# Kernel tuning notes

Hardware: AMD Instinct MI355X
Metric: run time of the kernel (lower is better)

## Reference

```python
import jax, jax.numpy as jnp
import numpy as np

D_MODEL = 1024
N_HEAD = 16


def setup_inputs() -> dict:
    key = jax.random.key(0)
    k1, k2, k3 = jax.random.split(key, 3)
    scale = 1.0 / np.sqrt(D_MODEL)
    x = jax.random.normal(k1, (1, 4096, D_MODEL), dtype=jnp.float32)
    # nn.Linear weights stored as [out, in]; applied as x @ W.T
    w_attn = jax.random.normal(k2, (3 * D_MODEL, D_MODEL), dtype=jnp.float32) * scale
    w_proj = jax.random.normal(k3, (D_MODEL, D_MODEL), dtype=jnp.float32) * scale
    return {"x": x, "w_attn": w_attn, "w_proj": w_proj}


def reference(x, w_attn, w_proj):
    B, T, C = x.shape
    H = N_HEAD
    hd = C // H
    qkv = x @ w_attn.T                      # [B, T, 3C]
    q, k, v = jnp.split(qkv, 3, axis=-1)
    # [B, T, C] -> [B, H, T, hd]
    q = q.reshape(B, T, H, hd).transpose(0, 2, 1, 3)
    k = k.reshape(B, T, H, hd).transpose(0, 2, 1, 3)
    v = v.reshape(B, T, H, hd).transpose(0, 2, 1, 3)
    att = jnp.einsum("bhqd,bhkd->bhqk", q, k) * (1.0 / np.sqrt(hd))  # [B,H,T,T]
    causal = jnp.tril(jnp.ones((T, T), dtype=bool))
    att = jnp.where(causal[None, None], att, -jnp.inf)
    att = jax.nn.softmax(att, axis=-1)
    y = jnp.einsum("bhqk,bhkd->bhqd", att, v)  # [B,H,T,hd]
    y = y.transpose(0, 2, 1, 3).reshape(B, T, C)
    return y @ w_proj.T
```

## Files before the change

### kernel.cpp

```cpp
#include <hip/hip_runtime.h>
#include <hip/hip_bf16.h>
#include <stdint.h>

typedef __bf16 bf16x8 __attribute__((ext_vector_type(8)));
typedef float f32x4 __attribute__((ext_vector_type(4)));

#define T_SEQ 4096
#define C_DIM 1024
#define H_NUM 16
#define HD 64
#define C3 3072
#define NEG_BIG (-30000.0f)

__device__ __forceinline__ unsigned short f2bf(float f) {
    uint32_t u = __builtin_bit_cast(uint32_t, f);
    u += 0x7fffu + ((u >> 16) & 1u);
    return (unsigned short)(u >> 16);
}

__device__ __forceinline__ uint32_t pk_bf16(float a, float b) {
    __hip_bfloat162 h = __float22bfloat162_rn(float2{a, b});
    uint32_t u;
    __builtin_memcpy(&u, &h, sizeof(u));
    return u;
}

__device__ __forceinline__ bf16x8 ld_bf8(const unsigned short* p) {
    return *reinterpret_cast<const bf16x8*>(p);
}

__device__ __forceinline__ void async_g2l16(const unsigned short* g, unsigned short* l) {
    __builtin_amdgcn_global_load_lds(
        (const __attribute__((address_space(1))) void*)g,
        (__attribute__((address_space(3))) void*)l, 16, 0, 0);
}

__device__ __forceinline__ void store_c(unsigned short* C, size_t idx, float v) { C[idx] = f2bf(v); }
__device__ __forceinline__ void store_c(float* C, size_t idx, float v)          { C[idx] = v; }

__device__ __forceinline__ void cvt8(const float* src, unsigned short* dst) {
    float4 f0 = *(const float4*)src;
    float4 f1 = *(const float4*)(src + 4);
    union { uint32_t w[4]; uint4 q; } t;
    t.w[0] = pk_bf16(f0.x, f0.y);
    t.w[1] = pk_bf16(f0.z, f0.w);
    t.w[2] = pk_bf16(f1.x, f1.y);
    t.w[3] = pk_bf16(f1.z, f1.w);
    *(uint4*)dst = t.q;
}

__global__ void cvt_xw(const float* __restrict__ x, const float* __restrict__ wa,
                       unsigned short* __restrict__ xb, unsigned short* __restrict__ wab) {
    int i = (blockIdx.x * blockDim.x + threadIdx.x) * 8;
    if (i < T_SEQ * C_DIM) cvt8(x + i, xb + i);
    else {
        int k = i - T_SEQ * C_DIM;
        if (k < C3 * C_DIM) cvt8(wa + k, wab + k);
    }
}

__global__ void cvt_f32_bf16(const float* __restrict__ src, unsigned short* __restrict__ dst, int n) {
    int i = (blockIdx.x * blockDim.x + threadIdx.x) * 8;
    if (i >= n) return;
    cvt8(src + i, dst + i);
}

__global__ __launch_bounds__(256) void v_transpose(
    const unsigned short* __restrict__ qkv, unsigned short* __restrict__ Vt)
{
    __shared__ unsigned short tile[64][72];
    const int t0 = blockIdx.x * 64, c0 = blockIdx.y * 64;
    const int r = threadIdx.x >> 2, q = threadIdx.x & 3;

    const unsigned short* src = qkv + (size_t)(t0 + r) * C3 + 2 * C_DIM + c0 + q * 16;
    *(uint4*)&tile[r][q * 16]     = *(const uint4*)src;
    *(uint4*)&tile[r][q * 16 + 8] = *(const uint4*)(src + 8);
    __syncthreads();

    union { unsigned short u[16]; uint4 v[2]; } o;
    #pragma unroll
    for (int j = 0; j < 16; ++j) o.u[j] = tile[q * 16 + j][r];
    unsigned short* dst = Vt + (size_t)(c0 + r) * T_SEQ + t0 + q * 16;
    *(uint4*)dst       = o.v[0];
    *(uint4*)(dst + 8) = o.v[1];
}

template <typename TC>
__global__ __launch_bounds__(256, 2) void gemm_bt(
    const unsigned short* __restrict__ A, const unsigned short* __restrict__ B,
    TC* __restrict__ C, int M, int N, int K)
{
    __shared__ __attribute__((aligned(16))) unsigned short As[128 * 32];
    __shared__ __attribute__((aligned(16))) unsigned short Bs[128 * 32];

    const int tid  = threadIdx.x;
    const int wave = tid >> 6, lane = tid & 63;
    const int quad = lane >> 4, l16 = lane & 15;
    const int wm = wave >> 1, wn = wave & 1;
    const int m0 = blockIdx.y * 128, n0 = blockIdx.x * 128;

    const int srow = wave * 32 + (lane >> 2);
    const int scol = (lane & 3) * 8;

    f32x4 acc[4][4] = {};

    for (int k0 = 0; k0 < K; k0 += 32) {
        {
            const unsigned short* ga = A + (size_t)(m0 + srow) * K + k0 + scol;
            const unsigned short* gb = B + (size_t)(n0 + srow) * K + k0 + scol;
            unsigned short* la = As + (wave * 32) * 32;
            unsigned short* lb = Bs + (wave * 32) * 32;
            async_g2l16(ga, la);
            async_g2l16(ga + (size_t)16 * K, la + 16 * 32);
            async_g2l16(gb, lb);
            async_g2l16(gb + (size_t)16 * K, lb + 16 * 32);
        }
        __syncthreads();

        bf16x8 af[4], bf[4];
        #pragma unroll
        for (int i = 0; i < 4; ++i) {
            af[i] = ld_bf8(As + (wm * 64 + i * 16 + l16) * 32 + quad * 8);
            bf[i] = ld_bf8(Bs + (wn * 64 + i * 16 + l16) * 32 + quad * 8);
        }
        #pragma unroll
        for (int mt = 0; mt < 4; ++mt)
            #pragma unroll
            for (int nt = 0; nt < 4; ++nt)
                acc[mt][nt] = __builtin_amdgcn_mfma_f32_16x16x32_bf16(
                    af[mt], bf[nt], acc[mt][nt], 0, 0, 0);
        __syncthreads();
    }

    #pragma unroll
    for (int mt = 0; mt < 4; ++mt)
        #pragma unroll
        for (int nt = 0; nt < 4; ++nt)
            #pragma unroll
            for (int r = 0; r < 4; ++r) {
                int row = m0 + wm * 64 + mt * 16 + quad * 4 + r;
                int col = n0 + wn * 64 + nt * 16 + l16;
                store_c(C, (size_t)row * N + col, acc[mt][nt][r]);
            }
}

#if __has_builtin(__builtin_amdgcn_permlane32_swap) && __has_builtin(__builtin_amdgcn_permlane16_swap)
#define HAVE_PERMLANE_SWAP 1
#else
#define HAVE_PERMLANE_SWAP 0
#endif

__device__ __forceinline__ void quad_xpose_pair(uint32_t X, uint32_t Y,
                                                uint32_t& t0, uint32_t& t1) {
#if HAVE_PERMLANE_SWAP
    auto S = __builtin_amdgcn_permlane32_swap((int)X, (int)Y, false, false);
    auto T = __builtin_amdgcn_permlane16_swap((int)S[0], (int)S[1], false, false);
    t0 = (uint32_t)T[0];
    t1 = (uint32_t)T[1];
#else
    const unsigned l = threadIdx.x & 63;
    uint32_t Ys = (uint32_t)__shfl_xor((int)Y, 32, 64);
    uint32_t Xs = (uint32_t)__shfl_xor((int)X, 32, 64);
    uint32_t S0 = (l < 32) ? X : Ys;
    uint32_t S1 = (l < 32) ? Xs : Y;
    uint32_t S0s = (uint32_t)__shfl_xor((int)S0, 16, 64);
    uint32_t S1s = (uint32_t)__shfl_xor((int)S1, 16, 64);
    t0 = (l & 16) ? S1s : S0;
    t1 = (l & 16) ? S1 : S0s;
#endif
}

template <bool MASK>
__device__ __forceinline__ void fa7_tile(
    const unsigned short* Ksb, const unsigned short* Vsb,
    const bf16x8 qf[2][2], f32x4 o[2][4], float* l_part,
    int k0, int q_abs0, int quad, int l16, int fo0, int fo1)
{
    const unsigned short* krow = Ksb + l16 * 64;
    bf16x8 kf[4][2];
    #pragma unroll
    for (int s = 0; s < 4; ++s) {
        kf[s][0] = ld_bf8(krow + s * 1024 + fo0);
        kf[s][1] = ld_bf8(krow + s * 1024 + fo1);
    }

    bf16x8 pf[2][2];
    #pragma unroll
    for (int qs = 0; qs < 2; ++qs) {
        f32x4 st[4];
        __builtin_amdgcn_s_setprio(1);
        #pragma unroll
        for (int s = 0; s < 4; ++s) {
            f32x4 z = {};
            z = __builtin_amdgcn_mfma_f32_16x16x32_bf16(kf[s][0], qf[qs][0], z, 0, 0, 0);
            st[s] = __builtin_amdgcn_mfma_f32_16x16x32_bf16(kf[s][1], qf[qs][1], z, 0, 0, 0);
        }
        __builtin_amdgcn_s_setprio(0);

        float ts = 0.f;
        #pragma unroll
        for (int s = 0; s < 4; ++s)
            #pragma unroll
            for (int r = 0; r < 4; ++r) {
                float v = st[s][r];
                if (MASK) {
                    int key = k0 + s * 16 + quad * 4 + r;
                    v = (key <= q_abs0 + qs * 16) ? v : NEG_BIG;
                }
                float e = __builtin_amdgcn_exp2f(v);
                st[s][r] = e;
                ts += e;
            }
        l_part[qs] += ts;

        uint32_t W[4][2];
        #pragma unroll
        for (int s = 0; s < 4; ++s) {
            W[s][0] = pk_bf16(st[s][0], st[s][1]);
            W[s][1] = pk_bf16(st[s][2], st[s][3]);
        }
        union { uint32_t w[4]; bf16x8 v; } pA, pB;
        quad_xpose_pair(W[0][0], W[1][0], pA.w[0], pA.w[2]);
        quad_xpose_pair(W[0][1], W[1][1], pA.w[1], pA.w[3]);
        quad_xpose_pair(W[2][0], W[3][0], pB.w[0], pB.w[2]);
        quad_xpose_pair(W[2][1], W[3][1], pB.w[1], pB.w[3]);
        pf[qs][0] = pA.v;
        pf[qs][1] = pB.v;
    }

    const unsigned short* vrow = Vsb + l16 * 64;
    bf16x8 vf[4][2];
    #pragma unroll
    for (int c = 0; c < 4; ++c) {
        vf[c][0] = ld_bf8(vrow + c * 1024 + fo0);
        vf[c][1] = ld_bf8(vrow + c * 1024 + fo1);
    }
    __builtin_amdgcn_s_setprio(1);
    #pragma unroll
    for (int qs = 0; qs < 2; ++qs)
        #pragma unroll
        for (int c = 0; c < 4; ++c) {
            o[qs][c] = __builtin_amdgcn_mfma_f32_16x16x32_bf16(vf[c][0], pf[qs][0], o[qs][c], 0, 0, 0);
            o[qs][c] = __builtin_amdgcn_mfma_f32_16x16x32_bf16(vf[c][1], pf[qs][1], o[qs][c], 0, 0, 0);
        }
    __builtin_amdgcn_s_setprio(0);
}

__global__ __launch_bounds__(128, 2) void flash_attn7(
    const unsigned short* __restrict__ qkv,
    const unsigned short* __restrict__ Vt,
    unsigned short* __restrict__ Y)
{
    __shared__ __attribute__((aligned(16))) unsigned short Ks[2][64 * 64];
    __shared__ __attribute__((aligned(16))) unsigned short Vs[2][64 * 64];

    const int tid  = threadIdx.x;
    const int wave = tid >> 6, lane = tid & 63;
    const int quad = lane >> 4, l16 = lane & 15;

    const int bi = blockIdx.x;
    const int rr = bi >> 8, ss = bi & 255;
    const int h  = ss & 15;
    const int j  = ss >> 4;
    const int qb = (rr == 0) ? j : (rr == 1) ? 63 - j : (rr == 2) ? 16 + j : 47 - j;

    const int q0w    = qb * 64 + wave * 32;
    const int q_abs0 = q0w + l16;
    const int sw  = l16 & 7;
    const int fo0 = (quad ^ sw) * 8;
    const int fo1 = ((quad + 4) ^ sw) * 8;

    bf16x8 qf[2][2];
    {
        const float QS = 0.125f * 1.44269504f;
        #pragma unroll
        for (int qs = 0; qs < 2; ++qs) {
            const unsigned short* qp =
                qkv + (size_t)(q0w + qs * 16 + l16) * C3 + h * HD + quad * 8;
            bf16x8 a = ld_bf8(qp), b = ld_bf8(qp + 32);
            #pragma unroll
            for (int i = 0; i < 8; ++i) {
                qf[qs][0][i] = (__bf16)((float)a[i] * QS);
                qf[qs][1][i] = (__bf16)((float)b[i] * QS);
            }
        }
    }

    const int srow = lane >> 3;
    const int schunk = (lane & 7) ^ srow;
    const unsigned short* kp =
        qkv + (size_t)(wave * 32 + srow) * C3 + C_DIM + h * HD + schunk * 8;
    const unsigned short* vp =
        Vt + (size_t)(h * HD + wave * 32 + srow) * T_SEQ + schunk * 8;
    unsigned short* lk = Ks[0] + (wave * 32) * 64;
    unsigned short* lv = Vs[0] + (wave * 32) * 64;
    const int lds_db = 64 * 64;
    const size_t kstep = (size_t)8 * C3;
    const size_t vstep = (size_t)8 * T_SEQ;

    auto stage = [&](int b) {
        #pragma unroll
        for (int jj = 0; jj < 4; ++jj) {
            async_g2l16(kp + jj * kstep, lk + b * lds_db + jj * 8 * 64);
            async_g2l16(vp + jj * vstep, lv + b * lds_db + jj * 8 * 64);
        }
    };

    f32x4 o[2][4] = {};
    float l_part[2] = {0.f, 0.f};

    const int ntiles = qb + 1;
    stage(0);
    kp += (size_t)64 * C3; vp += 64;

    for (int t = 0; t < ntiles; ++t) {
        __syncthreads();
        const int b = t & 1;
        if (t + 1 < ntiles) {
            stage(1 - b);
            kp += (size_t)64 * C3; vp += 64;
            fa7_tile<false>(Ks[b], Vs[b], qf, o, l_part,
                            t * 64, q_abs0, quad, l16, fo0, fo1);
        } else {
            fa7_tile<true>(Ks[b], Vs[b], qf, o, l_part,
                           t * 64, q_abs0, quad, l16, fo0, fo1);
        }
    }

    #pragma unroll
    for (int qs = 0; qs < 2; ++qs) {
        float l = l_part[qs];
        l += __shfl_xor(l, 16, 64);
        l += __shfl_xor(l, 32, 64);
        float inv_l = 1.f / l;
        #pragma unroll
        for (int c = 0; c < 4; ++c) {
            union { uint32_t w[2]; uint2 q; } t;
            t.w[0] = pk_bf16(o[qs][c][0] * inv_l, o[qs][c][1] * inv_l);
            t.w[1] = pk_bf16(o[qs][c][2] * inv_l, o[qs][c][3] * inv_l);
            *(uint2*)(Y + (size_t)(q_abs0 + qs * 16) * C_DIM + h * HD + c * 16 + quad * 4) = t.q;
        }
    }
}

extern "C" void kernel_launch(void* const* d_in, const int* in_sizes, int n_in,
                              void* d_out, int out_size, void* d_ws, size_t ws_size,
                              hipStream_t stream) {
    const float* x      = (const float*)d_in[0];
    const float* w_attn = (const float*)d_in[1];
    const float* w_proj = (const float*)d_in[2];
    float* out = (float*)d_out;

    unsigned short* qkv = (unsigned short*)d_ws;
    unsigned short* xb  = qkv + (size_t)T_SEQ * C3;
    unsigned short* y   = xb;
    unsigned short* wpb = qkv;
    unsigned short* Vt  = (unsigned short*)d_out;
    unsigned short* wab = Vt + (size_t)C_DIM * T_SEQ;

    cvt_xw<<<(T_SEQ * C_DIM + C3 * C_DIM) / 8 / 256, 256, 0, stream>>>(x, w_attn, xb, wab);

    gemm_bt<unsigned short>
        <<<dim3(C3 / 128, T_SEQ / 128), 256, 0, stream>>>(xb, wab, qkv, T_SEQ, C3, C_DIM);

    v_transpose<<<dim3(T_SEQ / 64, C_DIM / 64), 256, 0, stream>>>(qkv, Vt);

    flash_attn7<<<dim3(1024), 128, 0, stream>>>(qkv, Vt, y);

    cvt_f32_bf16<<<(C_DIM * C_DIM / 8 + 255) / 256, 256, 0, stream>>>(w_proj, wpb, C_DIM * C_DIM);
    gemm_bt<float>
        <<<dim3(C_DIM / 128, T_SEQ / 128), 256, 0, stream>>>(y, wpb, out, T_SEQ, C_DIM, C_DIM);
}
```

Before: 220.8 us.

## Split KV tiles across two wave pairs per block with LDS reduction

The attention kernel now launches 256-thread blocks in which two wave pairs process alternating 64-key tiles for the same query block, so each block walks roughly half as many rounds. Each round stages two K/V tiles at once into double-buffered LDS. The two partial outputs and row sums are then combined through LDS before normalisation. Block scheduling also changes to a simple longest-first query order. This shortens the serial KV loop per block at the cost of doubled LDS, an extra reduction step and possible idle waves on odd tile counts.

Measured after the change: 198.5 us. -10.1%, faster.

```diff
diff --git a/kernel.cpp b/kernel.cpp
--- a/kernel.cpp
+++ b/kernel.cpp
@@ -246,25 +246,24 @@
     __builtin_amdgcn_s_setprio(0);
 }
 
-__global__ __launch_bounds__(128, 2) void flash_attn7(
+__global__ __launch_bounds__(256, 2) void flash_attn8(
     const unsigned short* __restrict__ qkv,
     const unsigned short* __restrict__ Vt,
     unsigned short* __restrict__ Y)
 {
-    __shared__ __attribute__((aligned(16))) unsigned short Ks[2][64 * 64];
-    __shared__ __attribute__((aligned(16))) unsigned short Vs[2][64 * 64];
+    __shared__ __attribute__((aligned(16))) unsigned short Ks[2][2][4096];
+    __shared__ __attribute__((aligned(16))) unsigned short Vs[2][2][4096];
 
     const int tid  = threadIdx.x;
     const int wave = tid >> 6, lane = tid & 63;
     const int quad = lane >> 4, l16 = lane & 15;
+    const int wq = wave >> 1, wk = wave & 1;
 
     const int bi = blockIdx.x;
-    const int rr = bi >> 8, ss = bi & 255;
-    const int h  = ss & 15;
-    const int j  = ss >> 4;
-    const int qb = (rr == 0) ? j : (rr == 1) ? 63 - j : (rr == 2) ? 16 + j : 47 - j;
-
-    const int q0w    = qb * 64 + wave * 32;
+    const int h  = bi & 15;
+    const int qb = (bi < 512) ? (63 - (bi >> 4)) : (31 - ((bi - 512) >> 4));
+
+    const int q0w    = qb * 64 + wq * 32;
     const int q_abs0 = q0w + l16;
     const int sw  = l16 & 7;
     const int fo0 = (quad ^ sw) * 8;
@@ -286,15 +285,15 @@
         }
     }
 
-    const int srow = lane >> 3;
+    const int srow   = lane >> 3;
     const int schunk = (lane & 7) ^ srow;
     const unsigned short* kp =
-        qkv + (size_t)(wave * 32 + srow) * C3 + C_DIM + h * HD + schunk * 8;
+        qkv + (size_t)(wq * 64 + wk * 32 + srow) * C3 + C_DIM + h * HD + schunk * 8;
     const unsigned short* vp =
-        Vt + (size_t)(h * HD + wave * 32 + srow) * T_SEQ + schunk * 8;
-    unsigned short* lk = Ks[0] + (wave * 32) * 64;
-    unsigned short* lv = Vs[0] + (wave * 32) * 64;
-    const int lds_db = 64 * 64;
+        Vt + (size_t)(h * HD + wk * 32 + srow) * T_SEQ + wq * 64 + schunk * 8;
+    unsigned short* lk = &Ks[0][wq][(wk * 32) * 64];
+    unsigned short* lv = &Vs[0][wq][(wk * 32) * 64];
+    const int lds_db = 2 * 4096;
     const size_t kstep = (size_t)8 * C3;
     const size_t vstep = (size_t)8 * T_SEQ;
 
@@ -309,36 +308,66 @@
     f32x4 o[2][4] = {};
     float l_part[2] = {0.f, 0.f};
 
-    const int ntiles = qb + 1;
+    const int nt = qb + 1;
+    const int R  = (nt + 1) >> 1;
     stage(0);
-    kp += (size_t)64 * C3; vp += 64;
-
-    for (int t = 0; t < ntiles; ++t) {
+    kp += (size_t)128 * C3; vp += 128;
+
+    for (int r = 0; r < R; ++r) {
         __syncthreads();
-        const int b = t & 1;
-        if (t + 1 < ntiles) {
+        const int b = r & 1;
+        if (r + 1 < R) {
             stage(1 - b);
-            kp += (size_t)64 * C3; vp += 64;
-            fa7_tile<false>(Ks[b], Vs[b], qf, o, l_part,
-                            t * 64, q_abs0, quad, l16, fo0, fo1);
-        } else {
-            fa7_tile<true>(Ks[b], Vs[b], qf, o, l_part,
-                           t * 64, q_abs0, quad, l16, fo0, fo1);
-        }
-    }
-
-    #pragma unroll
-    for (int qs = 0; qs < 2; ++qs) {
-        float l = l_part[qs];
-        l += __shfl_xor(l, 16, 64);
-        l += __shfl_xor(l, 32, 64);
-        float inv_l = 1.f / l;
-        #pragma unroll
-        for (int c = 0; c < 4; ++c) {
-            union { uint32_t w[2]; uint2 q; } t;
-            t.w[0] = pk_bf16(o[qs][c][0] * inv_l, o[qs][c][1] * inv_l);
-            t.w[1] = pk_bf16(o[qs][c][2] * inv_l, o[qs][c][3] * inv_l);
-            *(uint2*)(Y + (size_t)(q_abs0 + qs * 16) * C_DIM + h * HD + c * 16 + quad * 4) = t.q;
+            kp += (size_t)128 * C3; vp += 128;
+        }
+        const int t = 2 * r + wk;
+        if (t < nt) {
+            if (t == nt - 1)
+                fa7_tile<true>(&Ks[b][wk][0], &Vs[b][wk][0], qf, o, l_part,
+                               t * 64, q_abs0, quad, l16, fo0, fo1);
+            else
+                fa7_tile<false>(&Ks[b][wk][0], &Vs[b][wk][0], qf, o, l_part,
+                                t * 64, q_abs0, quad, l16, fo0, fo1);
+        }
+    }
+
+    __syncthreads();
+    float* red  = (float*)&Ks[0][0][0];
+    float* lred = (float*)&Vs[0][0][0];
+    if (wk == 1) {
+        #pragma unroll
+        for (int qs = 0; qs < 2; ++qs)
+            #pragma unroll
+            for (int c = 0; c < 4; ++c)
+                *(f32x4*)&red[((wq * 8 + qs * 4 + c) * 64 + lane) * 4] = o[qs][c];
+        lred[wq * 128 + lane * 2 + 0] = l_part[0];
+        lred[wq * 128 + lane * 2 + 1] = l_part[1];
+    }
+    __syncthreads();
+    if (wk == 0) {
+        #pragma unroll
+        for (int qs = 0; qs < 2; ++qs) {
+            #pragma unroll
+            for (int c = 0; c < 4; ++c) {
+                f32x4 p = *(f32x4*)&red[((wq * 8 + qs * 4 + c) * 64 + lane) * 4];
+                o[qs][c] += p;
+            }
+            l_part[qs] += lred[wq * 128 + lane * 2 + qs];
+        }
+
+        #pragma unroll
+        for (int qs = 0; qs < 2; ++qs) {
+            float l = l_part[qs];
+            l += __shfl_xor(l, 16, 64);
+            l += __shfl_xor(l, 32, 64);
+            float inv_l = 1.f / l;
+            #pragma unroll
+            for (int c = 0; c < 4; ++c) {
+                union { uint32_t w[2]; uint2 q; } t;
+                t.w[0] = pk_bf16(o[qs][c][0] * inv_l, o[qs][c][1] * inv_l);
+                t.w[1] = pk_bf16(o[qs][c][2] * inv_l, o[qs][c][3] * inv_l);
+                *(uint2*)(Y + (size_t)(q_abs0 + qs * 16) * C_DIM + h * HD + c * 16 + quad * 4) = t.q;
+            }
         }
     }
 }
@@ -365,7 +394,7 @@
 
     v_transpose<<<dim3(T_SEQ / 64, C_DIM / 64), 256, 0, stream>>>(qkv, Vt);
 
-    flash_attn7<<<dim3(1024), 128, 0, stream>>>(qkv, Vt, y);
+    flash_attn8<<<dim3(1024), 256, 0, stream>>>(qkv, Vt, y);
 
     cvt_f32_bf16<<<(C_DIM * C_DIM / 8 + 255) / 256, 256, 0, stream>>>(w_proj, wpb, C_DIM * C_DIM);
     gemm_bt<float>
```
